# Performance work log

Hardware: AMD Instinct MI355X
Metric: run time of the kernel (lower is better)

## Reference

```python
import jax, jax.numpy as jnp
import numpy as np

EPS = 1e-8


def setup_inputs() -> dict:
    key = jax.random.key(0)
    k1, k2 = jax.random.split(key)
    N, D = 2048, 1024
    source = jax.random.normal(k1, (N, D), dtype=jnp.float32)
    target = jax.random.normal(k2, (N, D), dtype=jnp.float32)
    return {"source": source, "target": target}


def reference(source, target):
    N = source.shape[0]
    total = jnp.concatenate([source, target], axis=0)          # [2N, D]
    # Pairwise squared L2 via Gram trick: ||a||^2 + ||b||^2 - 2 a.b
    sq = jnp.sum(total * total, axis=-1)                       # [2N]
    gram = total @ total.T                                     # [2N, 2N]
    L2 = jnp.maximum(sq[:, None] + sq[None, :] - 2.0 * gram, 0.0)
    # torch.median on even-length flat array returns the LOWER of the two
    # middle elements, i.e. sorted[(numel - 1) // 2]
    flat = jnp.sort(L2.ravel())
    median_l2 = flat[(flat.size - 1) // 2]
    log_n = jnp.log(jnp.float32(N) + EPS)
    bandwidth = jax.lax.stop_gradient(jnp.sqrt(0.5 * median_l2 / log_n))
    kernel = jnp.exp(-L2 / (2.0 * bandwidth ** 2))             # [2N, 2N]
    XX = kernel[:N, :N]
    YY = kernel[N:, N:]
    XY = kernel[:N, N:]
    YX = kernel[N:, :N]
    loss = jnp.mean(XX + YY - XY - YX)
    return loss, bandwidth
```

## Files before the change

### kernel.cpp

```cpp
#include <hip/hip_runtime.h>

typedef unsigned int uint;
typedef unsigned short ushort;
using short8 = __attribute__((ext_vector_type(8))) short;
using f32x4  = __attribute__((ext_vector_type(4))) float;

#define NHALF 2048
#define DIM   1024
#define MROWS 4096
#define KMED  8388607u
#define NTRI  136

#define AH_OFF   0ull
#define SQ_OFF   8388608ull
#define GHT_OFF  (SQ_OFF + 16384ull)
#define GHN_OFF  (GHT_OFF + 65600ull)
#define CNT_OFF  (GHN_OFF + 65600ull)
#define ZERO_WORDS 32804

#define AGLOAD(p) __hip_atomic_load((p), __ATOMIC_RELAXED, __HIP_MEMORY_SCOPE_AGENT)

__device__ __forceinline__ ushort f2bf(float x) {
    uint u = __float_as_uint(x);
    u += 0x7FFFu + ((u >> 16) & 1u);
    return (ushort)(u >> 16);
}

__global__ __launch_bounds__(256) void convert_kernel(const float* __restrict__ src,
                                                      const float* __restrict__ tgt,
                                                      char* __restrict__ wsb) {
    ushort* ah = (ushort*)(wsb + AH_OFF);
    float*  sq = (float*)(wsb + SQ_OFF);
    uint*   z  = (uint*)(wsb + GHT_OFF);
    int t = threadIdx.x, row = blockIdx.x;
    int g = row * 256 + t;
    if (g < ZERO_WORDS) z[g] = 0;
    const float* p = (row < NHALF) ? src + (size_t)row * DIM
                                   : tgt + (size_t)(row - NHALF) * DIM;
    float4 v = reinterpret_cast<const float4*>(p)[t];
    float xs[4] = {v.x, v.y, v.z, v.w};
    ushort hh[4];
    float s = 0.0f;
#pragma unroll
    for (int e = 0; e < 4; ++e) { float x = xs[e]; s += x * x; hh[e] = f2bf(x); }
    ushort4 h4; h4.x = hh[0]; h4.y = hh[1]; h4.z = hh[2]; h4.w = hh[3];
    reinterpret_cast<ushort4*>(ah + (size_t)row * DIM)[t] = h4;
    for (int o = 32; o; o >>= 1) s += __shfl_down(s, o);
    __shared__ float red[4];
    if ((t & 63) == 0) red[t >> 6] = s;
    __syncthreads();
    if (t == 0) sq[row] = red[0] + red[1] + red[2] + red[3];
}

#define STAGEU(buf, u, kt) do {                                                            \
    int _arr = (u) >> 1;                                                                   \
    int _rb  = _arr ? colbase : rowbase;                                                   \
    _Pragma("unroll")                                                                      \
    for (int _l = 0; _l < 2; ++_l) {                                                       \
        int _r0 = ((u) & 1) * 128 + (wid * 2 + _l) * 8;                                    \
        const ushort* _g = ah + (size_t)(_rb + _r0 + (lane >> 3)) * DIM                    \
                           + (kt) * 64 + (((lane & 7) ^ (lane >> 3)) * 8);                 \
        __builtin_amdgcn_global_load_lds(                                                  \
            (const __attribute__((address_space(1))) uint*)_g,                             \
            (__attribute__((address_space(3))) uint*)(&lds[buf][_arr][0][0] + (size_t)_r0 * 64), \
            16, 0, 0);                                                                     \
    }                                                                                      \
} while (0)

#define RD(arr, lrow, ks) \
    (*reinterpret_cast<const short8*>(&lds[cur][arr][0][0] + (size_t)(lrow) * 64 + \
        (((ks) * 4 + fkk) ^ (fr & 7)) * 8))

__global__ __launch_bounds__(512, 2) void gemm_kernel(char* __restrict__ wsb,
                                                      float* __restrict__ out) {
    const ushort* ah = (const ushort*)(wsb + AH_OFF);
    const float*  sq = (const float*)(wsb + SQ_OFF);
    uint*  ght = (uint*)(wsb + GHT_OFF);
    uint*  ghn = (uint*)(wsb + GHN_OFF);
    uint*  cnt = (uint*)(wsb + CNT_OFF);

    __shared__ __align__(16) ushort lds[2][2][256][64];
    __shared__ uint lowcnt;
    __shared__ float fred[8];

    int b = (int)blockIdx.x;
    b = (b & 7) * 17 + (b >> 3);
    int bi = (int)((sqrtf(8.0f * (float)b + 1.0f) - 1.0f) * 0.5f);
    while ((bi + 1) * (bi + 2) / 2 <= b) ++bi;
    while (bi * (bi + 1) / 2 > b) --bi;
    int bj = b - bi * (bi + 1) / 2;

    int t = threadIdx.x;
    int lane = t & 63, wid = t >> 6;
    int wm = wid >> 2, wn = wid & 3;
    int rowbase = bi * 256, colbase = bj * 256;

    f32x4 acc[8][4] = {};
    int fr = lane & 15, fkk = lane >> 4;

    STAGEU(0, 0, 0); STAGEU(0, 1, 0); STAGEU(0, 2, 0); STAGEU(0, 3, 0);

    short8 fa[4][2], fb[4][2];

    for (int kt = 0; kt < 16; ++kt) {
        int cur = kt & 1, nxt = cur ^ 1;
        bool st = kt < 15;
        if (st) {
            STAGEU(nxt, 0, kt + 1);
            asm volatile("s_waitcnt vmcnt(2)" ::: "memory");
        } else {
            asm volatile("s_waitcnt vmcnt(0)" ::: "memory");
        }
        __builtin_amdgcn_s_barrier();
#pragma unroll
        for (int mi = 0; mi < 4; ++mi)
#pragma unroll
            for (int ks = 0; ks < 2; ++ks)
                fa[mi][ks] = RD(0, wm * 128 + mi * 16 + fr, ks);
#pragma unroll
        for (int ni = 0; ni < 2; ++ni)
#pragma unroll
            for (int ks = 0; ks < 2; ++ks)
                fb[ni][ks] = RD(1, wn * 64 + ni * 16 + fr, ks);
        __builtin_amdgcn_s_setprio(1);
#pragma unroll
        for (int mi = 0; mi < 4; ++mi)
#pragma unroll
            for (int ni = 0; ni < 2; ++ni)
#pragma unroll
                for (int ks = 0; ks < 2; ++ks)
                    acc[mi][ni] = __builtin_amdgcn_mfma_f32_16x16x32_bf16(fa[mi][ks], fb[ni][ks], acc[mi][ni], 0, 0, 0);
        __builtin_amdgcn_s_setprio(0);
        __builtin_amdgcn_s_barrier();
        if (st) STAGEU(nxt, 1, kt + 1);
        __builtin_amdgcn_s_barrier();
#pragma unroll
        for (int ni = 0; ni < 2; ++ni)
#pragma unroll
            for (int ks = 0; ks < 2; ++ks)
                fb[2 + ni][ks] = RD(1, wn * 64 + 32 + ni * 16 + fr, ks);
        __builtin_amdgcn_s_setprio(1);
#pragma unroll
        for (int mi = 0; mi < 4; ++mi)
#pragma unroll
            for (int ni = 0; ni < 2; ++ni)
#pragma unroll
                for (int ks = 0; ks < 2; ++ks)
                    acc[mi][2 + ni] = __builtin_amdgcn_mfma_f32_16x16x32_bf16(fa[mi][ks], fb[2 + ni][ks], acc[mi][2 + ni], 0, 0, 0);
        __builtin_amdgcn_s_setprio(0);
        __builtin_amdgcn_s_barrier();
        if (st) STAGEU(nxt, 2, kt + 1);
        __builtin_amdgcn_s_barrier();
#pragma unroll
        for (int mi = 0; mi < 4; ++mi)
#pragma unroll
            for (int ks = 0; ks < 2; ++ks)
                fa[mi][ks] = RD(0, wm * 128 + 64 + mi * 16 + fr, ks);
        __builtin_amdgcn_s_setprio(1);
#pragma unroll
        for (int mi = 0; mi < 4; ++mi)
#pragma unroll
            for (int ni = 0; ni < 2; ++ni)
#pragma unroll
                for (int ks = 0; ks < 2; ++ks)
                    acc[4 + mi][2 + ni] = __builtin_amdgcn_mfma_f32_16x16x32_bf16(fa[mi][ks], fb[2 + ni][ks], acc[4 + mi][2 + ni], 0, 0, 0);
        __builtin_amdgcn_s_setprio(0);
        __builtin_amdgcn_s_barrier();
        if (st) STAGEU(nxt, 3, kt + 1);
        __builtin_amdgcn_s_barrier();
        __builtin_amdgcn_s_setprio(1);
#pragma unroll
        for (int mi = 0; mi < 4; ++mi)
#pragma unroll
            for (int ni = 0; ni < 2; ++ni)
#pragma unroll
                for (int ks = 0; ks < 2; ++ks)
                    acc[4 + mi][ni] = __builtin_amdgcn_mfma_f32_16x16x32_bf16(fa[mi][ks], fb[ni][ks], acc[4 + mi][ni], 0, 0, 0);
        __builtin_amdgcn_s_setprio(0);
        __builtin_amdgcn_s_barrier();
    }
    __syncthreads();

    uint* h = (uint*)&lds[0][0][0][0];
    for (int i = t; i < 8192; i += 512) h[i] = 0;
    if (t == 0) lowcnt = 0;
    __syncthreads();

    uint w = (bi == bj) ? 1u : 2u;
    int fq = fkk;
#pragma unroll
    for (int mi = 0; mi < 8; ++mi) {
#pragma unroll
        for (int ni = 0; ni < 4; ++ni) {
            int gj = colbase + wn * 64 + ni * 16 + fr;
            float sqj = sq[gj];
#pragma unroll
            for (int r = 0; r < 4; ++r) {
                int gi = rowbase + wm * 128 + mi * 16 + fq * 4 + r;
                float v = fmaxf(sq[gi] + sqj - 2.0f * acc[mi][ni][r], 0.0f);
                uint bits = __float_as_uint(v);
                if (bits & 0x40000000u) {
                    uint k14 = (bits >> 16) & 0x3FFFu;
                    atomicAdd(&h[k14 >> 1], (k14 & 1) ? (w << 16) : w);
                } else {
                    atomicAdd(&lowcnt, w);
                }
            }
        }
    }
    __syncthreads();

    bool crosshalf = (bi < 8) != (bj < 8);
    for (int i = t; i < 8192; i += 512) {
        uint wd = h[i];
        if (wd) {
            uint lo = wd & 0xFFFFu, hi2 = wd >> 16;
            if (lo)  { atomicAdd(&ght[2 * i],     lo);  if (crosshalf) atomicAdd(&ghn[2 * i],     lo); }
            if (hi2) { atomicAdd(&ght[2 * i + 1], hi2); if (crosshalf) atomicAdd(&ghn[2 * i + 1], hi2); }
        }
    }
    if (t == 0 && lowcnt) {
        atomicAdd(&ght[16384], lowcnt);
        if (crosshalf) atomicAdd(&ghn[16384], lowcnt);
    }

    __syncthreads();
    if (t == 0) {
        __threadfence();
        h[0] = (atomicAdd(&cnt[0], 1u) == gridDim.x - 1) ? 1u : 0u;
    }
    __syncthreads();
    bool last = h[0] != 0;
    __syncthreads();
    if (!last) return;

    uint* part = h + 16;
    uint* loc  = h + 544;
    uint* lin  = h + 560;
    uint s = 0;
    for (int i = 0; i < 32; ++i) s += AGLOAD(&ght[t * 32 + i]);
    part[t] = s;
    __syncthreads();
    if (t == 0) {
        uint k = KMED - AGLOAD(&ght[16384]);
        uint cum = 0; int seg = 0;
        for (; seg < 512; ++seg) { uint c = part[seg]; if (cum + c > k) break; cum += c; }
        loc[0] = (uint)seg; loc[1] = k - cum;
    }
    __syncthreads();
    int seg = (int)loc[0];
    if (t < 32) lin[t] = AGLOAD(&ght[seg * 32 + t]);
    __syncthreads();
    if (t == 0) {
        uint k = loc[1], cum = 0; int bb = 0;
        for (; bb < 32; ++bb) { uint c = lin[bb]; if (cum + c > k) break; cum += c; }
        uint mbits = 0x40000000u | ((uint)(seg * 32 + bb) << 16) | 0x8000u;
        float median = __uint_as_float(mbits);
        float logn = logf(2048.0f + 1e-8f);
        float bw = sqrtf(0.5f * median / logn);
        out[1] = bw;
        ((float*)loc)[1] = logn / median;
    }
    __syncthreads();
    float itb = ((float*)loc)[1];

    float local = 0.0f;
    for (int i = 0; i < 32; ++i) {
        int bidx = t * 32 + i;
        int tot = (int)AGLOAD(&ght[bidx]);
        int neg = (int)AGLOAD(&ghn[bidx]);
        int sgn = tot - 2 * neg;
        if (sgn) {
            float mid = __uint_as_float(0x40000000u | ((uint)bidx << 16) | 0x8000u);
            local += (float)sgn * __expf(-mid * itb);
        }
    }
    if (t == 0)
        local += (float)((int)AGLOAD(&ght[16384]) - 2 * (int)AGLOAD(&ghn[16384]));
    for (int o = 32; o; o >>= 1) local += __shfl_down(local, o);
    if ((t & 63) == 0) fred[t >> 6] = local;
    __syncthreads();
    if (t == 0) {
        float bs = fred[0] + fred[1] + fred[2] + fred[3]
                 + fred[4] + fred[5] + fred[6] + fred[7];
        out[0] = bs / 4194304.0f;
    }
}

extern "C" void kernel_launch(void* const* d_in, const int* in_sizes, int n_in,
                              void* d_out, int out_size, void* d_ws, size_t ws_size,
                              hipStream_t stream) {
    const float* src = (const float*)d_in[0];
    const float* tgt = (const float*)d_in[1];
    float* out = (float*)d_out;
    char* ws = (char*)d_ws;

    convert_kernel<<<MROWS, 256, 0, stream>>>(src, tgt, ws);
    gemm_kernel<<<NTRI, 512, 0, stream>>>(ws, out);
}
```

Measured before the change: 83.49 us.

## Split symmetric Gram tiles into 256x128 blocks with 1024-thread workgroups

Changes the lower-triangle tiling from 136 blocks of 256x256 to 272 blocks of 256x128, each run by 1024 threads (16 waves) with smaller per-wave accumulators. Diagonal handling moves from whole-tile weights to per-element weighting (2 below the diagonal, 1 on it, skip above). The aim is to fill more of the 256 CUs and balance work better. In exchange it loads more redundant A data relative to compute, caps occupancy at one workgroup per CU, and redoes the last-block histogram scan with 1024 threads.

```diff
diff --git a/kernel.cpp b/kernel.cpp
--- a/kernel.cpp
+++ b/kernel.cpp
@@ -9,7 +9,7 @@
 #define DIM   1024
 #define MROWS 4096
 #define KMED  8388607u
-#define NTRI  136
+#define NTRI  272
 
 #define AH_OFF   0ull
 #define SQ_OFF   8388608ull
@@ -52,151 +52,137 @@
     if (t == 0) sq[row] = red[0] + red[1] + red[2] + red[3];
 }
 
-#define STAGEU(buf, u, kt) do {                                                            \
-    int _arr = (u) >> 1;                                                                   \
-    int _rb  = _arr ? colbase : rowbase;                                                   \
-    _Pragma("unroll")                                                                      \
-    for (int _l = 0; _l < 2; ++_l) {                                                       \
-        int _r0 = ((u) & 1) * 128 + (wid * 2 + _l) * 8;                                    \
-        const ushort* _g = ah + (size_t)(_rb + _r0 + (lane >> 3)) * DIM                    \
-                           + (kt) * 64 + (((lane & 7) ^ (lane >> 3)) * 8);                 \
-        __builtin_amdgcn_global_load_lds(                                                  \
-            (const __attribute__((address_space(1))) uint*)_g,                             \
-            (__attribute__((address_space(3))) uint*)(&lds[buf][_arr][0][0] + (size_t)_r0 * 64), \
-            16, 0, 0);                                                                     \
-    }                                                                                      \
+#define STAGEA(buf, u, kt) do {                                                            \
+    const ushort* _g = ah + (size_t)(rowbase + (u) * 128 + wid * 8 + (lane >> 3)) * DIM    \
+                       + (kt) * 64 + (((lane & 7) ^ ((lane >> 3) & 7)) * 8);               \
+    __builtin_amdgcn_global_load_lds(                                                      \
+        (const __attribute__((address_space(1))) uint*)_g,                                 \
+        (__attribute__((address_space(3))) uint*)(ldsb + (buf) * 24576 + ((u) * 128 + wid * 8) * 64), \
+        16, 0, 0);                                                                         \
 } while (0)
-
-#define RD(arr, lrow, ks) \
-    (*reinterpret_cast<const short8*>(&lds[cur][arr][0][0] + (size_t)(lrow) * 64 + \
-        (((ks) * 4 + fkk) ^ (fr & 7)) * 8))
-
-__global__ __launch_bounds__(512, 2) void gemm_kernel(char* __restrict__ wsb,
-                                                      float* __restrict__ out) {
+#define STAGEB(buf, kt) do {                                                               \
+    const ushort* _g = ah + (size_t)(colbase + wid * 8 + (lane >> 3)) * DIM                \
+                       + (kt) * 64 + (((lane & 7) ^ ((lane >> 3) & 7)) * 8);               \
+    __builtin_amdgcn_global_load_lds(                                                      \
+        (const __attribute__((address_space(1))) uint*)_g,                                 \
+        (__attribute__((address_space(3))) uint*)(ldsb + (buf) * 24576 + (256 + wid * 8) * 64), \
+        16, 0, 0);                                                                         \
+} while (0)
+
+#define RDA(lrow, ks) (*reinterpret_cast<const short8*>(ldsb + cur * 24576 + (size_t)(lrow) * 64 + \
+        ((((ks) * 4 + fkk) ^ (fr & 7)) * 8)))
+#define RDB(lrow, ks) (*reinterpret_cast<const short8*>(ldsb + cur * 24576 + 16384 + (size_t)(lrow) * 64 + \
+        ((((ks) * 4 + fkk) ^ (fr & 7)) * 8)))
+
+__global__ __launch_bounds__(1024, 1) void gemm_kernel(char* __restrict__ wsb,
+                                                       float* __restrict__ out) {
     const ushort* ah = (const ushort*)(wsb + AH_OFF);
     const float*  sq = (const float*)(wsb + SQ_OFF);
     uint*  ght = (uint*)(wsb + GHT_OFF);
     uint*  ghn = (uint*)(wsb + GHN_OFF);
     uint*  cnt = (uint*)(wsb + CNT_OFF);
 
-    __shared__ __align__(16) ushort lds[2][2][256][64];
+    __shared__ __align__(16) ushort lds[2][24576];
     __shared__ uint lowcnt;
-    __shared__ float fred[8];
+    __shared__ float fred[16];
+    ushort* ldsb = &lds[0][0];
 
     int b = (int)blockIdx.x;
-    b = (b & 7) * 17 + (b >> 3);
-    int bi = (int)((sqrtf(8.0f * (float)b + 1.0f) - 1.0f) * 0.5f);
-    while ((bi + 1) * (bi + 2) / 2 <= b) ++bi;
-    while (bi * (bi + 1) / 2 > b) --bi;
-    int bj = b - bi * (bi + 1) / 2;
+    b = (b & 7) * 34 + (b >> 3);
+    int ri = (int)((sqrtf(4.0f * (float)b + 1.0f) - 1.0f) * 0.5f);
+    while ((ri + 1) * (ri + 2) <= b) ++ri;
+    while (ri * (ri + 1) > b) --ri;
+    int cj = b - ri * (ri + 1);
+    int rowbase = ri * 256, colbase = cj * 128;
 
     int t = threadIdx.x;
     int lane = t & 63, wid = t >> 6;
     int wm = wid >> 2, wn = wid & 3;
-    int rowbase = bi * 256, colbase = bj * 256;
-
-    f32x4 acc[8][4] = {};
+    f32x4 acc[4][2] = {};
     int fr = lane & 15, fkk = lane >> 4;
 
-    STAGEU(0, 0, 0); STAGEU(0, 1, 0); STAGEU(0, 2, 0); STAGEU(0, 3, 0);
-
-    short8 fa[4][2], fb[4][2];
+    STAGEA(0, 0, 0); STAGEA(0, 1, 0); STAGEB(0, 0);
+
+    short8 fa[2][2], fa2[2][2], fb0[2], fb1[2];
 
     for (int kt = 0; kt < 16; ++kt) {
         int cur = kt & 1, nxt = cur ^ 1;
         bool st = kt < 15;
-        if (st) {
-            STAGEU(nxt, 0, kt + 1);
-            asm volatile("s_waitcnt vmcnt(2)" ::: "memory");
-        } else {
-            asm volatile("s_waitcnt vmcnt(0)" ::: "memory");
-        }
-        __builtin_amdgcn_s_barrier();
-#pragma unroll
-        for (int mi = 0; mi < 4; ++mi)
-#pragma unroll
-            for (int ks = 0; ks < 2; ++ks)
-                fa[mi][ks] = RD(0, wm * 128 + mi * 16 + fr, ks);
-#pragma unroll
-        for (int ni = 0; ni < 2; ++ni)
-#pragma unroll
-            for (int ks = 0; ks < 2; ++ks)
-                fb[ni][ks] = RD(1, wn * 64 + ni * 16 + fr, ks);
-        __builtin_amdgcn_s_setprio(1);
-#pragma unroll
-        for (int mi = 0; mi < 4; ++mi)
-#pragma unroll
-            for (int ni = 0; ni < 2; ++ni)
-#pragma unroll
-                for (int ks = 0; ks < 2; ++ks)
-                    acc[mi][ni] = __builtin_amdgcn_mfma_f32_16x16x32_bf16(fa[mi][ks], fb[ni][ks], acc[mi][ni], 0, 0, 0);
-        __builtin_amdgcn_s_setprio(0);
-        __builtin_amdgcn_s_barrier();
-        if (st) STAGEU(nxt, 1, kt + 1);
-        __builtin_amdgcn_s_barrier();
-#pragma unroll
-        for (int ni = 0; ni < 2; ++ni)
-#pragma unroll
-            for (int ks = 0; ks < 2; ++ks)
-                fb[2 + ni][ks] = RD(1, wn * 64 + 32 + ni * 16 + fr, ks);
-        __builtin_amdgcn_s_setprio(1);
-#pragma unroll
-        for (int mi = 0; mi < 4; ++mi)
-#pragma unroll
-            for (int ni = 0; ni < 2; ++ni)
-#pragma unroll
-                for (int ks = 0; ks < 2; ++ks)
-                    acc[mi][2 + ni] = __builtin_amdgcn_mfma_f32_16x16x32_bf16(fa[mi][ks], fb[2 + ni][ks], acc[mi][2 + ni], 0, 0, 0);
-        __builtin_amdgcn_s_setprio(0);
-        __builtin_amdgcn_s_barrier();
-        if (st) STAGEU(nxt, 2, kt + 1);
-        __builtin_amdgcn_s_barrier();
-#pragma unroll
-        for (int mi = 0; mi < 4; ++mi)
-#pragma unroll
-            for (int ks = 0; ks < 2; ++ks)
-                fa[mi][ks] = RD(0, wm * 128 + 64 + mi * 16 + fr, ks);
-        __builtin_amdgcn_s_setprio(1);
-#pragma unroll
-        for (int mi = 0; mi < 4; ++mi)
-#pragma unroll
-            for (int ni = 0; ni < 2; ++ni)
-#pragma unroll
-                for (int ks = 0; ks < 2; ++ks)
-                    acc[4 + mi][2 + ni] = __builtin_amdgcn_mfma_f32_16x16x32_bf16(fa[mi][ks], fb[2 + ni][ks], acc[4 + mi][2 + ni], 0, 0, 0);
-        __builtin_amdgcn_s_setprio(0);
-        __builtin_amdgcn_s_barrier();
-        if (st) STAGEU(nxt, 3, kt + 1);
-        __builtin_amdgcn_s_barrier();
-        __builtin_amdgcn_s_setprio(1);
-#pragma unroll
-        for (int mi = 0; mi < 4; ++mi)
-#pragma unroll
-            for (int ni = 0; ni < 2; ++ni)
-#pragma unroll
-                for (int ks = 0; ks < 2; ++ks)
-                    acc[4 + mi][ni] = __builtin_amdgcn_mfma_f32_16x16x32_bf16(fa[mi][ks], fb[ni][ks], acc[4 + mi][ni], 0, 0, 0);
-        __builtin_amdgcn_s_setprio(0);
-        __builtin_amdgcn_s_barrier();
-    }
-    __syncthreads();
-
-    uint* h = (uint*)&lds[0][0][0][0];
-    for (int i = t; i < 8192; i += 512) h[i] = 0;
+        if (st) { STAGEA(nxt, 0, kt + 1); asm volatile("s_waitcnt vmcnt(1)" ::: "memory"); }
+        else    { asm volatile("s_waitcnt vmcnt(0)" ::: "memory"); }
+        __builtin_amdgcn_s_barrier();
+#pragma unroll
+        for (int mi = 0; mi < 2; ++mi)
+#pragma unroll
+            for (int ks = 0; ks < 2; ++ks)
+                fa[mi][ks] = RDA(wm * 64 + mi * 16 + fr, ks);
+#pragma unroll
+        for (int ks = 0; ks < 2; ++ks)
+            fb0[ks] = RDB(wn * 32 + fr, ks);
+        __builtin_amdgcn_s_setprio(1);
+#pragma unroll
+        for (int mi = 0; mi < 2; ++mi)
+#pragma unroll
+            for (int ks = 0; ks < 2; ++ks)
+                acc[mi][0] = __builtin_amdgcn_mfma_f32_16x16x32_bf16(fa[mi][ks], fb0[ks], acc[mi][0], 0, 0, 0);
+        __builtin_amdgcn_s_setprio(0);
+        __builtin_amdgcn_s_barrier();
+        if (st) STAGEA(nxt, 1, kt + 1);
+        __builtin_amdgcn_s_barrier();
+#pragma unroll
+        for (int ks = 0; ks < 2; ++ks)
+            fb1[ks] = RDB(wn * 32 + 16 + fr, ks);
+        __builtin_amdgcn_s_setprio(1);
+#pragma unroll
+        for (int mi = 0; mi < 2; ++mi)
+#pragma unroll
+            for (int ks = 0; ks < 2; ++ks)
+                acc[mi][1] = __builtin_amdgcn_mfma_f32_16x16x32_bf16(fa[mi][ks], fb1[ks], acc[mi][1], 0, 0, 0);
+        __builtin_amdgcn_s_setprio(0);
+        __builtin_amdgcn_s_barrier();
+        if (st) STAGEB(nxt, kt + 1);
+        __builtin_amdgcn_s_barrier();
+#pragma unroll
+        for (int mi = 0; mi < 2; ++mi)
+#pragma unroll
+            for (int ks = 0; ks < 2; ++ks)
+                fa2[mi][ks] = RDA(wm * 64 + 32 + mi * 16 + fr, ks);
+        __builtin_amdgcn_s_setprio(1);
+#pragma unroll
+        for (int mi = 0; mi < 2; ++mi)
+#pragma unroll
+            for (int ks = 0; ks < 2; ++ks)
+                acc[2 + mi][1] = __builtin_amdgcn_mfma_f32_16x16x32_bf16(fa2[mi][ks], fb1[ks], acc[2 + mi][1], 0, 0, 0);
+        __builtin_amdgcn_s_setprio(0);
+        __builtin_amdgcn_s_barrier();
+        __builtin_amdgcn_s_setprio(1);
+#pragma unroll
+        for (int mi = 0; mi < 2; ++mi)
+#pragma unroll
+            for (int ks = 0; ks < 2; ++ks)
+                acc[2 + mi][0] = __builtin_amdgcn_mfma_f32_16x16x32_bf16(fa2[mi][ks], fb0[ks], acc[2 + mi][0], 0, 0, 0);
+        __builtin_amdgcn_s_setprio(0);
+        __builtin_amdgcn_s_barrier();
+    }
+    __syncthreads();
+
+    uint* h = (uint*)ldsb;
+    for (int i = t; i < 8192; i += 1024) h[i] = 0;
     if (t == 0) lowcnt = 0;
     __syncthreads();
 
-    uint w = (bi == bj) ? 1u : 2u;
     int fq = fkk;
 #pragma unroll
-    for (int mi = 0; mi < 8; ++mi) {
-#pragma unroll
-        for (int ni = 0; ni < 4; ++ni) {
-            int gj = colbase + wn * 64 + ni * 16 + fr;
+    for (int mi = 0; mi < 4; ++mi) {
+#pragma unroll
+        for (int ni = 0; ni < 2; ++ni) {
+            int gj = colbase + wn * 32 + ni * 16 + fr;
             float sqj = sq[gj];
 #pragma unroll
             for (int r = 0; r < 4; ++r) {
-                int gi = rowbase + wm * 128 + mi * 16 + fq * 4 + r;
+                int gi = rowbase + wm * 64 + mi * 16 + fq * 4 + r;
+                uint w = (gj < gi) ? 2u : ((gj == gi) ? 1u : 0u);
+                if (!w) continue;
                 float v = fmaxf(sq[gi] + sqj - 2.0f * acc[mi][ni][r], 0.0f);
                 uint bits = __float_as_uint(v);
                 if (bits & 0x40000000u) {
@@ -210,8 +196,8 @@
     }
     __syncthreads();
 
-    bool crosshalf = (bi < 8) != (bj < 8);
-    for (int i = t; i < 8192; i += 512) {
+    bool crosshalf = (ri < 8) != (cj < 16);
+    for (int i = t; i < 8192; i += 1024) {
         uint wd = h[i];
         if (wd) {
             uint lo = wd & 0xFFFFu, hi2 = wd >> 16;
@@ -235,26 +221,26 @@
     if (!last) return;
 
     uint* part = h + 16;
-    uint* loc  = h + 544;
-    uint* lin  = h + 560;
+    uint* loc  = h + 1056;
+    uint* lin  = h + 1072;
     uint s = 0;
-    for (int i = 0; i < 32; ++i) s += AGLOAD(&ght[t * 32 + i]);
+    for (int i = 0; i < 16; ++i) s += AGLOAD(&ght[t * 16 + i]);
     part[t] = s;
     __syncthreads();
     if (t == 0) {
         uint k = KMED - AGLOAD(&ght[16384]);
         uint cum = 0; int seg = 0;
-        for (; seg < 512; ++seg) { uint c = part[seg]; if (cum + c > k) break; cum += c; }
+        for (; seg < 1024; ++seg) { uint c = part[seg]; if (cum + c > k) break; cum += c; }
         loc[0] = (uint)seg; loc[1] = k - cum;
     }
     __syncthreads();
     int seg = (int)loc[0];
-    if (t < 32) lin[t] = AGLOAD(&ght[seg * 32 + t]);
+    if (t < 16) lin[t] = AGLOAD(&ght[seg * 16 + t]);
     __syncthreads();
     if (t == 0) {
         uint k = loc[1], cum = 0; int bb = 0;
-        for (; bb < 32; ++bb) { uint c = lin[bb]; if (cum + c > k) break; cum += c; }
-        uint mbits = 0x40000000u | ((uint)(seg * 32 + bb) << 16) | 0x8000u;
+        for (; bb < 16; ++bb) { uint c = lin[bb]; if (cum + c > k) break; cum += c; }
+        uint mbits = 0x40000000u | ((uint)(seg * 16 + bb) << 16) | 0x8000u;
         float median = __uint_as_float(mbits);
         float logn = logf(2048.0f + 1e-8f);
         float bw = sqrtf(0.5f * median / logn);
@@ -265,8 +251,8 @@
     float itb = ((float*)loc)[1];
 
     float local = 0.0f;
-    for (int i = 0; i < 32; ++i) {
-        int bidx = t * 32 + i;
+    for (int i = 0; i < 16; ++i) {
+        int bidx = t * 16 + i;
         int tot = (int)AGLOAD(&ght[bidx]);
         int neg = (int)AGLOAD(&ghn[bidx]);
         int sgn = tot - 2 * neg;
@@ -281,8 +267,9 @@
     if ((t & 63) == 0) fred[t >> 6] = local;
     __syncthreads();
     if (t == 0) {
-        float bs = fred[0] + fred[1] + fred[2] + fred[3]
-                 + fred[4] + fred[5] + fred[6] + fred[7];
+        float bs = 0.0f;
+#pragma unroll
+        for (int i = 0; i < 16; ++i) bs += fred[i];
         out[0] = bs / 4194304.0f;
     }
 }
@@ -296,5 +283,5 @@
     char* ws = (char*)d_ws;
 
     convert_kernel<<<MROWS, 256, 0, stream>>>(src, tgt, ws);
-    gemm_kernel<<<NTRI, 512, 0, stream>>>(ws, out);
-}
+    gemm_kernel<<<NTRI, 1024, 0, stream>>>(ws, out);
+}
```

Measured after the change: 101.5 us. +21.6%, slower.
